# Performance work log

Hardware: AMD Instinct MI355X
Metric: run time of the kernel (lower is better)

The kernel has to match this reference:

```python
import jax, jax.numpy as jnp
import numpy as np

N_NODES = 100000
N_EDGES = 1600000
D_FEAT = 128


def setup_inputs() -> dict:
    key = jax.random.key(0)
    k1, k2, k3 = jax.random.split(key, 3)
    x = jax.random.normal(k1, (N_NODES, D_FEAT), dtype=jnp.float32)
    src = jax.random.randint(k2, (N_EDGES,), 0, N_NODES, dtype=jnp.int64)
    dst = jax.random.randint(k3, (N_EDGES,), 0, N_NODES, dtype=jnp.int64)
    return {"x": x, "src": src, "dst": dst}


def reference(x, src, dst):
    # x: [N, D] node features; src/dst: [E] edge endpoints (edge u->v is src->dst)
    n = x.shape[0]
    # out-degree of every node (clamped to >= 1), matching graph.out_degrees()
    deg = jax.ops.segment_sum(jnp.ones(src.shape[0], dtype=x.dtype), src,
                              num_segments=n)
    deg = jnp.maximum(deg, jnp.asarray(1.0, dtype=x.dtype))
    # per-edge norm: 1/sqrt(deg_out(u) * deg_out(v))  (u_mul_v of out-degrees)
    norm = jax.lax.rsqrt(deg[src] * deg[dst])  # [E]
    # gather-multiply-scatter-sum: out[v] = sum_{(u->v)} x[u] * norm(u,v)
    msg = x[src] * norm[:, None]  # [E, D]
    return jax.ops.segment_sum(msg, dst, num_segments=n)
```

## Files before the change

### kernel.cpp

```cpp
#include <hip/hip_runtime.h>
#include <hip/hip_fp16.h>


#define D_FEAT 128
#define CAP 32
#define NODES_PER_BLOCK 8
#define SS_NODES 50000
#define SS_INTS  12500
#define SC_NODES 25000
#define SC_INTS   6250
#define PCLAMP   200

typedef float f32x4 __attribute__((ext_vector_type(4)));
typedef int   i32x4 __attribute__((ext_vector_type(4)));


__global__ void hist_kernel(const int* __restrict__ src, const int* __restrict__ dst,
                            unsigned* __restrict__ H, int E, int N,
                            int nss, int chunkSz, int nc) {
    int bid = blockIdx.x;
    int ax = bid & 1;
    int ss = (bid >> 1) % nss;
    int c  = bid / (2 * nss);
    const int* __restrict__ arr = ax ? dst : src;

    __shared__ unsigned hp[SS_INTS];
    int lo = ss * SS_NODES;
    int span = min(N - lo, SS_NODES);
    for (int i = threadIdx.x; i < SS_INTS; i += blockDim.x) hp[i] = 0u;
    __syncthreads();

    int beg = c * chunkSz;
    int end = min(E, beg + chunkSz);
    int i = beg + (int)threadIdx.x * 4;
    for (; i + 3 < end; i += blockDim.x * 4) {
        int4 v = *reinterpret_cast<const int4*>(&arr[i]);
        unsigned o;
        o = (unsigned)(v.x - lo); if (o < (unsigned)span) atomicAdd(&hp[o >> 2], 1u << (8 * (o & 3)));
        o = (unsigned)(v.y - lo); if (o < (unsigned)span) atomicAdd(&hp[o >> 2], 1u << (8 * (o & 3)));
        o = (unsigned)(v.z - lo); if (o < (unsigned)span) atomicAdd(&hp[o >> 2], 1u << (8 * (o & 3)));
        o = (unsigned)(v.w - lo); if (o < (unsigned)span) atomicAdd(&hp[o >> 2], 1u << (8 * (o & 3)));
    }
    if (i < end) {
        for (int k = i; k < end; ++k) {
            unsigned o = (unsigned)(arr[k] - lo);
            if (o < (unsigned)span) atomicAdd(&hp[o >> 2], 1u << (8 * (o & 3)));
        }
    }
    __syncthreads();

    size_t base = ((size_t)(ax * nss + ss) * nc + c) * SS_INTS;
    for (int j = threadIdx.x; j < SS_INTS; j += blockDim.x)
        __builtin_nontemporal_store(hp[j], &H[base + j]);
}

__global__ void scan_kernel(unsigned* __restrict__ H, float* __restrict__ isd,
                            int* __restrict__ cnt, int N, int nss, int nc) {
    int total = nss * SS_INTS;
    int g = blockIdx.x * blockDim.x + threadIdx.x;
    if (g >= 2 * total) return;
    int ax = (g >= total) ? 1 : 0;
    int gg = g - ax * total;
    int ss = gg / SS_INTS;
    int i  = gg - ss * SS_INTS;
    int node0 = ss * SS_NODES + 4 * i;

    size_t base = ((size_t)(ax * nss + ss) * nc) * SS_INTS + i;

    if (ax == 0) {
        int s0 = 0, s1 = 0, s2 = 0, s3 = 0;
        for (int c = 0; c < nc; c += 8) {
            unsigned w[8];
            #pragma unroll
            for (int u = 0; u < 8; ++u) w[u] = H[base + (size_t)(c + u) * SS_INTS];
            #pragma unroll
            for (int u = 0; u < 8; ++u) {
                s0 += w[u] & 255; s1 += (w[u] >> 8) & 255;
                s2 += (w[u] >> 16) & 255; s3 += w[u] >> 24;
            }
        }
        if (node0 + 0 < N) isd[node0 + 0] = rsqrtf(fmaxf((float)s0, 1.0f));
        if (node0 + 1 < N) isd[node0 + 1] = rsqrtf(fmaxf((float)s1, 1.0f));
        if (node0 + 2 < N) isd[node0 + 2] = rsqrtf(fmaxf((float)s2, 1.0f));
        if (node0 + 3 < N) isd[node0 + 3] = rsqrtf(fmaxf((float)s3, 1.0f));
    } else {
        int r0 = 0, r1 = 0, r2 = 0, r3 = 0;
        for (int c = 0; c < nc; c += 8) {
            unsigned w[8];
            #pragma unroll
            for (int u = 0; u < 8; ++u) w[u] = H[base + (size_t)(c + u) * SS_INTS];
            #pragma unroll
            for (int u = 0; u < 8; ++u) {
                unsigned p = (unsigned)min(r0, PCLAMP) | ((unsigned)min(r1, PCLAMP) << 8) |
                             ((unsigned)min(r2, PCLAMP) << 16) | ((unsigned)min(r3, PCLAMP) << 24);
                H[base + (size_t)(c + u) * SS_INTS] = p;
                r0 += w[u] & 255; r1 += (w[u] >> 8) & 255;
                r2 += (w[u] >> 16) & 255; r3 += w[u] >> 24;
            }
        }
        if (node0 + 0 < N) cnt[node0 + 0] = r0;
        if (node0 + 1 < N) cnt[node0 + 1] = r1;
        if (node0 + 2 < N) cnt[node0 + 2] = r2;
        if (node0 + 3 < N) cnt[node0 + 3] = r3;
    }
}

__global__ void scatter_kernel(const int* __restrict__ src, const int* __restrict__ dst,
                               const unsigned* __restrict__ H,
                               int* __restrict__ bucket, int2* __restrict__ ovf,
                               int* __restrict__ novf, int E, int N,
                               int nss, int nsc, int chunkSz, int nc) {
    int bid = blockIdx.x;
    int s = bid % nsc;
    int c = bid / nsc;

    __shared__ unsigned lcp[SC_INTS];
    int lo = s * SC_NODES;
    int span = min(N - lo, SC_NODES);
    int ss = s >> 1;
    size_t base = ((size_t)(nss + ss) * nc + c) * SS_INTS + (size_t)(s & 1) * SC_INTS;
    for (int i = threadIdx.x; i < SC_INTS; i += blockDim.x)
        lcp[i] = __builtin_nontemporal_load(&H[base + i]);
    __syncthreads();

    int beg = c * chunkSz;
    int end = min(E, beg + chunkSz);
    int i = beg + (int)threadIdx.x * 4;
    for (; i + 3 < end; i += blockDim.x * 4) {
        i32x4 dv = __builtin_nontemporal_load(reinterpret_cast<const i32x4*>(&dst[i]));
        i32x4 sv = __builtin_nontemporal_load(reinterpret_cast<const i32x4*>(&src[i]));
        #pragma unroll
        for (int k = 0; k < 4; ++k) {
            int d  = dv[k];
            int sx = sv[k];
            unsigned o = (unsigned)(d - lo);
            if (o < (unsigned)span) {
                int sh = 8 * (o & 3);
                unsigned old = atomicAdd(&lcp[o >> 2], 1u << sh);
                int slot = (old >> sh) & 255;
                if (slot < CAP) {
                    bucket[d * CAP + slot] = sx;
                } else {
                    int ov = atomicAdd(novf, 1);
                    ovf[ov] = make_int2(sx, d);
                }
            }
        }
    }
    if (i < end) {
        for (int k = i; k < end; ++k) {
            int d  = dst[k];
            int sx = src[k];
            unsigned o = (unsigned)(d - lo);
            if (o < (unsigned)span) {
                int sh = 8 * (o & 3);
                unsigned old = atomicAdd(&lcp[o >> 2], 1u << sh);
                int slot = (old >> sh) & 255;
                if (slot < CAP) {
                    bucket[d * CAP + slot] = sx;
                } else {
                    int ov = atomicAdd(novf, 1);
                    ovf[ov] = make_int2(sx, d);
                }
            }
        }
    }
}

__global__ void cvt_kernel(const f32x4* __restrict__ x4,
                           ushort4* __restrict__ x16, int n4) {
    int i = blockIdx.x * blockDim.x + threadIdx.x;
    if (i < n4) {
        f32x4 v = __builtin_nontemporal_load(&x4[i]);
        ushort4 h;
        h.x = __half_as_ushort(__float2half_rn(v.x));
        h.y = __half_as_ushort(__float2half_rn(v.y));
        h.z = __half_as_ushort(__float2half_rn(v.z));
        h.w = __half_as_ushort(__float2half_rn(v.w));
        x16[i] = h;
    }
}

__global__ void gather_kernel(const ushort4* __restrict__ x16,
                              const int* __restrict__ cnt,
                              const int* __restrict__ bucket,
                              const float* __restrict__ isd,
                              f32x4* __restrict__ out4, int N) {
    __shared__ int   sh_idx[NODES_PER_BLOCK * CAP];
    __shared__ float sh_w[NODES_PER_BLOCK * CAP];
    int t = threadIdx.x;
    int node_slot = t >> 5;
    int lane = t & 31;
    int d = blockIdx.x * NODES_PER_BLOCK + node_slot;

    int c = 0;
    if (d < N) {
        c = min(cnt[d], CAP);
        if (lane < c) {
            int s = __builtin_nontemporal_load(&bucket[d * CAP + lane]);
            sh_idx[node_slot * CAP + lane] = s;
            sh_w[node_slot * CAP + lane] = isd[s];
        }
    }
    __syncthreads();
    if (d >= N) return;

    f32x4 acc = {0.f, 0.f, 0.f, 0.f};
    #pragma unroll 8
    for (int k = 0; k < c; ++k) {
        int s   = sh_idx[node_slot * CAP + k];
        float w = sh_w[node_slot * CAP + k];
        ushort4 v = x16[s * 32 + lane];
        acc.x += __half2float(__ushort_as_half(v.x)) * w;
        acc.y += __half2float(__ushort_as_half(v.y)) * w;
        acc.z += __half2float(__ushort_as_half(v.z)) * w;
        acc.w += __half2float(__ushort_as_half(v.w)) * w;
    }
    float wd = isd[d];
    acc.x *= wd; acc.y *= wd; acc.z *= wd; acc.w *= wd;
    __builtin_nontemporal_store(acc, &out4[d * 32 + lane]);
}

__global__ void overflow_kernel(const float* __restrict__ x,
                                const float* __restrict__ isd,
                                const int2* __restrict__ ovf,
                                const int* __restrict__ novf,
                                float* __restrict__ out) {
    int n = *novf;
    for (int e = blockIdx.x; e < n; e += gridDim.x) {
        int2 sd = ovf[e];
        float coef = isd[sd.x] * isd[sd.y];
        atomicAdd(&out[sd.y * D_FEAT + threadIdx.x],
                  x[sd.x * D_FEAT + threadIdx.x] * coef);
    }
}

__global__ void gather32_kernel(const float4* __restrict__ x4,
                                const int* __restrict__ cnt,
                                const int* __restrict__ bucket,
                                const float* __restrict__ isd,
                                float4* __restrict__ out4, int N) {
    __shared__ int   sh_idx[NODES_PER_BLOCK * CAP];
    __shared__ float sh_w[NODES_PER_BLOCK * CAP];
    int t = threadIdx.x;
    int node_slot = t >> 5;
    int lane = t & 31;
    int d = blockIdx.x * NODES_PER_BLOCK + node_slot;

    int c = 0;
    if (d < N) {
        c = min(cnt[d], CAP);
        if (lane < c) {
            int s = bucket[d * CAP + lane];
            sh_idx[node_slot * CAP + lane] = s;
            sh_w[node_slot * CAP + lane] = isd[s];
        }
    }
    __syncthreads();
    if (d >= N) return;

    float4 acc = {0.f, 0.f, 0.f, 0.f};
    #pragma unroll 4
    for (int k = 0; k < c; ++k) {
        int s   = sh_idx[node_slot * CAP + k];
        float w = sh_w[node_slot * CAP + k];
        float4 v = x4[s * 32 + lane];
        acc.x += v.x * w; acc.y += v.y * w;
        acc.z += v.z * w; acc.w += v.w * w;
    }
    float wd = isd[d];
    acc.x *= wd; acc.y *= wd; acc.z *= wd; acc.w *= wd;
    out4[d * 32 + lane] = acc;
}

#define NSLICES_T2 8
#define BPS 512

__global__ void build_kernel(const int* __restrict__ src, const int* __restrict__ dst,
                             int* __restrict__ deg, int* __restrict__ cnt,
                             int* __restrict__ bucket, int2* __restrict__ ovf,
                             int* __restrict__ novf, int E, int sliceSz) {
    int slice = blockIdx.x & (NSLICES_T2 - 1);
    int chunk = blockIdx.x >> 3;
    int lo = slice * sliceSz;
    int hi = lo + sliceSz;
    int chunkSz = (E + BPS - 1) / BPS;
    int beg = chunk * chunkSz;
    int end = min(E, beg + chunkSz);

    for (int i = beg + (int)threadIdx.x; i < end; i += blockDim.x) {
        int s = src[i];
        int d = dst[i];
        if (d >= lo && d < hi) {
            int slot = atomicAdd(&cnt[d], 1);
            if (slot < CAP) {
                bucket[d * CAP + slot] = s;
            } else {
                int o = atomicAdd(novf, 1);
                ovf[o] = make_int2(s, d);
            }
        }
        if (s >= lo && s < hi) {
            atomicAdd(&deg[s], 1);
        }
    }
}

__global__ void isd_kernel(const int* __restrict__ deg, float* __restrict__ isd, int N) {
    int i = blockIdx.x * blockDim.x + threadIdx.x;
    if (i < N) isd[i] = rsqrtf(fmaxf((float)deg[i], 1.0f));
}

__global__ void fb_degree_kernel(const int* __restrict__ src,
                                 float* __restrict__ deg, int E) {
    int i = blockIdx.x * blockDim.x + threadIdx.x;
    if (i < E) atomicAdd(&deg[src[i]], 1.0f);
}
__global__ void fb_inv_sqrt_kernel(float* __restrict__ deg, int N) {
    int i = blockIdx.x * blockDim.x + threadIdx.x;
    if (i < N) deg[i] = rsqrtf(fmaxf(deg[i], 1.0f));
}
__global__ void fb_scatter_kernel(const float* __restrict__ x,
                                  const int* __restrict__ src,
                                  const int* __restrict__ dst,
                                  const float* __restrict__ isd,
                                  float* __restrict__ out, int E) {
    int e = blockIdx.x;
    if (e >= E) return;
    int f = threadIdx.x;
    int s = src[e], d = dst[e];
    float coef = isd[s] * isd[d];
    atomicAdd(&out[(long)d * D_FEAT + f], x[(long)s * D_FEAT + f] * coef);
}

extern "C" void kernel_launch(void* const* d_in, const int* in_sizes, int n_in,
                              void* d_out, int out_size, void* d_ws, size_t ws_size,
                              hipStream_t stream) {
    const float* x   = (const float*)d_in[0];
    const int*   src = (const int*)d_in[1];
    const int*   dst = (const int*)d_in[2];
    float* out = (float*)d_out;

    int N = in_sizes[0] / D_FEAT;
    int E = in_sizes[1];

    int nss = (N + SS_NODES - 1) / SS_NODES;
    int nsc = (N + SC_NODES - 1) / SC_NODES;

    size_t x16Sz = (size_t)N * D_FEAT * 2;

    int nc = 128;
    size_t off_cnt, off_isd, off_misc, off_bucket, off_H, off_ovf, needed;
    for (;;) {
        size_t hSz = (size_t)2 * nss * nc * SS_INTS * 4;
        size_t uSz = hSz > x16Sz ? hSz : x16Sz;
        off_cnt    = 0;
        off_isd    = off_cnt + (size_t)N * 4;
        off_misc   = off_isd + (size_t)N * 4;
        off_bucket = off_misc + 64;
        off_H      = off_bucket + (size_t)N * CAP * 4;
        off_ovf    = off_H + uSz;
        needed     = off_ovf + (size_t)E * 8;
        if (ws_size >= needed || nc == 16) break;
        nc >>= 1;
    }

    if (ws_size >= needed) {
        char* ws = (char*)d_ws;
        int*      cnt    = (int*)(ws + off_cnt);
        float*    isd    = (float*)(ws + off_isd);
        int*      novf   = (int*)(ws + off_misc);
        int*      bucket = (int*)(ws + off_bucket);
        unsigned* H      = (unsigned*)(ws + off_H);
        ushort4*  x16    = (ushort4*)(ws + off_H);
        int2*     ovf    = (int2*)(ws + off_ovf);

        hipMemsetAsync(novf, 0, 16, stream);

        int chunkSz = (((E + nc - 1) / nc) + 3) & ~3;

        hist_kernel<<<2 * nss * nc, 256, 0, stream>>>(
            src, dst, H, E, N, nss, chunkSz, nc);
        scan_kernel<<<(2 * nss * SS_INTS + 255) / 256, 256, 0, stream>>>(
            H, isd, cnt, N, nss, nc);
        scatter_kernel<<<nsc * nc, 256, 0, stream>>>(
            src, dst, H, bucket, ovf, novf, E, N, nss, nsc, chunkSz, nc);
        int n4 = N * (D_FEAT / 4);
        cvt_kernel<<<(n4 + 255) / 256, 256, 0, stream>>>(
            (const f32x4*)x, x16, n4);
        gather_kernel<<<(N + NODES_PER_BLOCK - 1) / NODES_PER_BLOCK, 256, 0, stream>>>(
            x16, cnt, bucket, isd, (f32x4*)out, N);
        overflow_kernel<<<64, D_FEAT, 0, stream>>>(x, isd, ovf, novf, out);
        return;
    }

    size_t t2_deg    = 0;
    size_t t2_cnt    = t2_deg + (size_t)N * 4;
    size_t t2_isd    = t2_cnt + (size_t)N * 4;
    size_t t2_novf   = t2_isd + (size_t)N * 4;
    size_t t2_bucket = t2_novf + 16;
    size_t t2_ovf    = t2_bucket + (size_t)N * CAP * 4;
    size_t t2_needed = t2_ovf + (size_t)E * 8;

    if (ws_size >= t2_needed) {
        char* ws = (char*)d_ws;
        int*   deg    = (int*)(ws + t2_deg);
        int*   cnt    = (int*)(ws + t2_cnt);
        float* isd    = (float*)(ws + t2_isd);
        int*   novf   = (int*)(ws + t2_novf);
        int*   bucket = (int*)(ws + t2_bucket);
        int2*  ovf    = (int2*)(ws + t2_ovf);

        hipMemsetAsync(ws, 0, t2_novf + 16, stream);
        int sl = (N + NSLICES_T2 - 1) / NSLICES_T2;
        build_kernel<<<NSLICES_T2 * BPS, 256, 0, stream>>>(src, dst, deg, cnt,
                                                           bucket, ovf, novf, E, sl);
        isd_kernel<<<(N + 255) / 256, 256, 0, stream>>>(deg, isd, N);
        gather32_kernel<<<(N + NODES_PER_BLOCK - 1) / NODES_PER_BLOCK, 256, 0, stream>>>(
            (const float4*)x, cnt, bucket, isd, (float4*)out, N);
        overflow_kernel<<<64, D_FEAT, 0, stream>>>(x, isd, ovf, novf, out);
        return;
    }

    float* deg = (float*)d_ws;
    hipMemsetAsync(deg, 0, (size_t)N * sizeof(float), stream);
    hipMemsetAsync(out, 0, (size_t)out_size * sizeof(float), stream);
    fb_degree_kernel<<<(E + 255) / 256, 256, 0, stream>>>(src, deg, E);
    fb_inv_sqrt_kernel<<<(N + 255) / 256, 256, 0, stream>>>(deg, N);
    fb_scatter_kernel<<<E, D_FEAT, 0, stream>>>(x, src, dst, deg, out, E);
}
```

Before: 273.2 us.

## Fold fp16 conversion into histogram launch and drop memset launch

Adds extra blocks to the histogram kernel that convert x to fp16 into a separate workspace region, so the conversion overlaps the histogram pass and the standalone cvt launch is removed when the workspace is large enough. The overflow counter is now zeroed inside the scan kernel instead of through a memset. Nontemporal loads and stores on H and the edge arrays are replaced with plain ones. The cost is a larger workspace footprint and conversion blocks that compete with histogram blocks for bandwidth and CUs.

```diff
diff --git a/kernel.cpp b/kernel.cpp
--- a/kernel.cpp
+++ b/kernel.cpp
@@ -10,15 +10,31 @@
 #define SC_NODES 25000
 #define SC_INTS   6250
 #define PCLAMP   200
+#define CVTB     512
 
 typedef float f32x4 __attribute__((ext_vector_type(4)));
-typedef int   i32x4 __attribute__((ext_vector_type(4)));
 
 
 __global__ void hist_kernel(const int* __restrict__ src, const int* __restrict__ dst,
                             unsigned* __restrict__ H, int E, int N,
-                            int nss, int chunkSz, int nc) {
+                            int nss, int chunkSz, int nc, int histBlocks,
+                            const f32x4* __restrict__ x4,
+                            ushort4* __restrict__ x16, int n4) {
     int bid = blockIdx.x;
+    if (bid >= histBlocks) {
+        for (int i = (bid - histBlocks) * (int)blockDim.x + (int)threadIdx.x;
+             i < n4; i += CVTB * (int)blockDim.x) {
+            f32x4 v = __builtin_nontemporal_load(&x4[i]);
+            ushort4 h;
+            h.x = __half_as_ushort(__float2half_rn(v.x));
+            h.y = __half_as_ushort(__float2half_rn(v.y));
+            h.z = __half_as_ushort(__float2half_rn(v.z));
+            h.w = __half_as_ushort(__float2half_rn(v.w));
+            x16[i] = h;
+        }
+        return;
+    }
+
     int ax = bid & 1;
     int ss = (bid >> 1) % nss;
     int c  = bid / (2 * nss);
@@ -50,14 +66,15 @@
     __syncthreads();
 
     size_t base = ((size_t)(ax * nss + ss) * nc + c) * SS_INTS;
-    for (int j = threadIdx.x; j < SS_INTS; j += blockDim.x)
-        __builtin_nontemporal_store(hp[j], &H[base + j]);
+    for (int j = threadIdx.x; j < SS_INTS; j += blockDim.x) H[base + j] = hp[j];
 }
 
 __global__ void scan_kernel(unsigned* __restrict__ H, float* __restrict__ isd,
-                            int* __restrict__ cnt, int N, int nss, int nc) {
+                            int* __restrict__ cnt, int* __restrict__ novf,
+                            int N, int nss, int nc) {
     int total = nss * SS_INTS;
     int g = blockIdx.x * blockDim.x + threadIdx.x;
+    if (g == 0) *novf = 0;
     if (g >= 2 * total) return;
     int ax = (g >= total) ? 1 : 0;
     int gg = g - ax * total;
@@ -119,20 +136,19 @@
     int span = min(N - lo, SC_NODES);
     int ss = s >> 1;
     size_t base = ((size_t)(nss + ss) * nc + c) * SS_INTS + (size_t)(s & 1) * SC_INTS;
-    for (int i = threadIdx.x; i < SC_INTS; i += blockDim.x)
-        lcp[i] = __builtin_nontemporal_load(&H[base + i]);
+    for (int i = threadIdx.x; i < SC_INTS; i += blockDim.x) lcp[i] = H[base + i];
     __syncthreads();
 
     int beg = c * chunkSz;
     int end = min(E, beg + chunkSz);
     int i = beg + (int)threadIdx.x * 4;
     for (; i + 3 < end; i += blockDim.x * 4) {
-        i32x4 dv = __builtin_nontemporal_load(reinterpret_cast<const i32x4*>(&dst[i]));
-        i32x4 sv = __builtin_nontemporal_load(reinterpret_cast<const i32x4*>(&src[i]));
+        int4 dv = *reinterpret_cast<const int4*>(&dst[i]);
+        int4 sv = *reinterpret_cast<const int4*>(&src[i]);
         #pragma unroll
         for (int k = 0; k < 4; ++k) {
-            int d  = dv[k];
-            int sx = sv[k];
+            int d  = (&dv.x)[k];
+            int sx = (&sv.x)[k];
             unsigned o = (unsigned)(d - lo);
             if (o < (unsigned)span) {
                 int sh = 8 * (o & 3);
@@ -348,46 +364,65 @@
     int nsc = (N + SC_NODES - 1) / SC_NODES;
 
     size_t x16Sz = (size_t)N * D_FEAT * 2;
-
-    int nc = 128;
-    size_t off_cnt, off_isd, off_misc, off_bucket, off_H, off_ovf, needed;
-    for (;;) {
-        size_t hSz = (size_t)2 * nss * nc * SS_INTS * 4;
+    int n4 = N * (D_FEAT / 4);
+
+    int nc = 0, modeA = 0;
+    size_t off_cnt = 0, off_isd = 0, off_misc = 0, off_bucket = 0,
+           off_H = 0, off_x16 = 0, off_ovf = 0;
+    for (int tryNc = 128; tryNc >= 16 && nc == 0; tryNc >>= 1) {
+        size_t hSz = (size_t)2 * nss * tryNc * SS_INTS * 4;
+        size_t cA  = 0;
+        off_cnt    = cA;                         cA += (size_t)N * 4;
+        off_isd    = cA;                         cA += (size_t)N * 4;
+        off_misc   = cA;                         cA += 64;
+        off_bucket = cA;                         cA += (size_t)N * CAP * 4;
+        off_H      = cA;
+        size_t a_x16 = off_H + hSz;
+        size_t a_ovf = a_x16 + x16Sz;
+        size_t a_need = a_ovf + (size_t)E * 8;
+        if (ws_size >= a_need) {
+            nc = tryNc; modeA = 1; off_x16 = a_x16; off_ovf = a_ovf;
+            break;
+        }
         size_t uSz = hSz > x16Sz ? hSz : x16Sz;
-        off_cnt    = 0;
-        off_isd    = off_cnt + (size_t)N * 4;
-        off_misc   = off_isd + (size_t)N * 4;
-        off_bucket = off_misc + 64;
-        off_H      = off_bucket + (size_t)N * CAP * 4;
-        off_ovf    = off_H + uSz;
-        needed     = off_ovf + (size_t)E * 8;
-        if (ws_size >= needed || nc == 16) break;
-        nc >>= 1;
-    }
-
-    if (ws_size >= needed) {
+        size_t b_ovf = off_H + uSz;
+        size_t b_need = b_ovf + (size_t)E * 8;
+        if (ws_size >= b_need) {
+            nc = tryNc; modeA = 0; off_x16 = off_H; off_ovf = b_ovf;
+            break;
+        }
+    }
+
+    if (nc > 0) {
         char* ws = (char*)d_ws;
         int*      cnt    = (int*)(ws + off_cnt);
         float*    isd    = (float*)(ws + off_isd);
         int*      novf   = (int*)(ws + off_misc);
         int*      bucket = (int*)(ws + off_bucket);
         unsigned* H      = (unsigned*)(ws + off_H);
-        ushort4*  x16    = (ushort4*)(ws + off_H);
+        ushort4*  x16    = (ushort4*)(ws + off_x16);
         int2*     ovf    = (int2*)(ws + off_ovf);
 
-        hipMemsetAsync(novf, 0, 16, stream);
-
         int chunkSz = (((E + nc - 1) / nc) + 3) & ~3;
-
-        hist_kernel<<<2 * nss * nc, 256, 0, stream>>>(
-            src, dst, H, E, N, nss, chunkSz, nc);
+        int histBlocks = 2 * nss * nc;
+
+        if (modeA) {
+            hist_kernel<<<histBlocks + CVTB, 256, 0, stream>>>(
+                src, dst, H, E, N, nss, chunkSz, nc, histBlocks,
+                (const f32x4*)x, x16, n4);
+        } else {
+            hist_kernel<<<histBlocks, 256, 0, stream>>>(
+                src, dst, H, E, N, nss, chunkSz, nc, histBlocks,
+                (const f32x4*)x, x16, 0);
+        }
         scan_kernel<<<(2 * nss * SS_INTS + 255) / 256, 256, 0, stream>>>(
-            H, isd, cnt, N, nss, nc);
+            H, isd, cnt, novf, N, nss, nc);
         scatter_kernel<<<nsc * nc, 256, 0, stream>>>(
             src, dst, H, bucket, ovf, novf, E, N, nss, nsc, chunkSz, nc);
-        int n4 = N * (D_FEAT / 4);
-        cvt_kernel<<<(n4 + 255) / 256, 256, 0, stream>>>(
-            (const f32x4*)x, x16, n4);
+        if (!modeA) {
+            cvt_kernel<<<(n4 + 255) / 256, 256, 0, stream>>>(
+                (const f32x4*)x, x16, n4);
+        }
         gather_kernel<<<(N + NODES_PER_BLOCK - 1) / NODES_PER_BLOCK, 256, 0, stream>>>(
             x16, cnt, bucket, isd, (f32x4*)out, N);
         overflow_kernel<<<64, D_FEAT, 0, stream>>>(x, isd, ovf, novf, out);
```

Result: faster. 251.3 us (-8.0%).
